# Performance work log

Measured on AMD Instinct MI355X. Metric: run time of the kernel, lower is better.

## Reference

```python
import jax, jax.numpy as jnp
import numpy as np

B, R, C = 32, 32, 32
NB, NC = 2, 20
CH = 6 + 2 * (R + C) + 2 * NC      # 174 label channels
CHP = NB * CH                      # 348 pred channels


def setup_inputs() -> dict:
    key = jax.random.key(0)
    pred = jax.random.uniform(key, (B, R, C, CHP), dtype=jnp.float32)
    rng = np.random.default_rng(0)
    label = rng.random((B, R, C, CH)).astype(np.float32)
    # object flag: exactly 1.0 where a center exists (the code tests == 1)
    label[..., 0] = (rng.random((B, R, C)) < 0.15).astype(np.float32)
    # one-hot corner row / col pointers
    rc = rng.integers(0, R, (B, R, C))
    cc = rng.integers(0, C, (B, R, C))
    label[..., 6:6 + R] = np.eye(R, dtype=np.float32)[rc]
    label[..., 6 + R:6 + R + C] = np.eye(C, dtype=np.float32)[cc]
    return {"pred": pred, "label": jnp.asarray(label), "num_box": NB, "num_class": NC}


def _take(a, idx):
    # gather one channel per cell; idx: [B,R,C] int
    return jnp.take_along_axis(a, idx[..., None], axis=-1)[..., 0]


def _convbox_match(pred, label, nb, nc):
    Bs, Rs, Cs, ch = label.shape
    chp = pred.shape[-1]
    base = 6 + 2 * (Rs + Cs)
    f32 = pred.dtype
    b_idx = jnp.arange(Bs)[:, None, None]
    rowm = jnp.broadcast_to(jnp.arange(Rs)[None, :, None], (Bs, Rs, Cs))
    colm = jnp.broadcast_to(jnp.arange(Cs)[None, None, :], (Bs, Rs, Cs))
    flag = (label[..., 0] == 1.0)
    rowc = jnp.argmax(label[..., 6:6 + Rs], axis=-1)            # first index of one-hot
    colc = jnp.argmax(label[..., 6 + Rs:6 + Rs + Cs], axis=-1)
    Lc = label[b_idx, rowc, colc]   # [B,R,C,ch]  values at corner cell
    Pc = pred[b_idx, rowc, colc]    # [B,R,C,chp]

    # ground-truth box per cell
    xm_t = (label[..., 2] + colm) / Cs
    ym_t = (label[..., 3] + rowm) / Rs
    xc_t = (Lc[..., 4] + colc) / Cs
    yc_t = (Lc[..., 5] + rowc) / Rs
    tw = jnp.abs(xm_t - xc_t) * 2.0
    th = jnp.abs(ym_t - yc_t) * 2.0

    scores = []
    for i in range(nb):
        sm = base * nb + i * nc
        sc = (base + nc) * nb + i * nc
        cat = (jnp.sum((pred[..., sm:sm + nc] - label[..., base:base + nc]) ** 2, -1)
               + jnp.sum((Pc[..., sc:sc + nc] - Lc[..., base + nc:base + 2 * nc]) ** 2, -1))
        conn_m = (_take(pred, 6 * nb + i * (Rs + Cs) + rowc)
                  * _take(pred, 6 * nb + i * (Rs + Cs) + Rs + colc))
        conn_c = (_take(Pc, (6 + Rs + Cs) * nb + i * (Rs + Cs) + rowm)
                  * _take(Pc, (6 + Rs + Cs) * nb + i * (Rs + Cs) + Rs + colm))
        conn = (conn_m + conn_c) / 2.0
        # faithful to source: channel index literally offset by colm / rowm
        xm_p = _take(pred, (nb + i) * 2 + 0 + colm) / Cs
        ym_p = _take(pred, (nb + i) * 2 + 1 + rowm) / Rs
        xc_p = _take(Pc, (nb * 2 + i) * 2 + 0 + colc) / Cs
        yc_p = _take(Pc, (nb * 2 + i) * 2 + 1 + rowc) / Rs
        ow = jnp.abs(xm_p - xc_p) * 2.0
        oh = jnp.abs(ym_p - yc_p) * 2.0
        w = jnp.minimum(xm_p + ow / 2, xm_t + tw / 2) - jnp.maximum(xm_p - ow / 2, xm_t - tw / 2)
        h = jnp.minimum(ym_p + oh / 2, ym_t + th / 2) - jnp.maximum(ym_p - oh / 2, ym_t - th / 2)
        inter = jnp.where((w < 0) | (h < 0), 0.0, w * h)
        union = ow * oh + tw * th - inter
        iou = inter / union
        rmse = (xm_p - xm_t) ** 2 + (ym_p - ym_t) ** 2 + (ow - tw) ** 2 + (oh - th) ** 2
        scores.append(conn * (iou - rmse + 0.1) + 0.1 * (2.0 - cat))
    best = jnp.argmax(jnp.stack(scores, axis=-1), axis=-1)  # [B,R,C] (first max, matches strict > update)

    val = flag.astype(f32)
    pred_mask = jnp.zeros((Bs, Rs, Cs, chp), f32)
    label_mask = jnp.zeros((Bs, Rs, Cs, ch), f32)
    ar_rc = jnp.arange(Rs + Cs)
    ar_nc = jnp.arange(nc)
    two = jnp.array([0, 1])
    bb = best[..., None]
    for n, (rt, ct) in enumerate([(rowm, colm), (rowc, colc)]):
        pch = jnp.concatenate([
            n * nb + bb,
            ((1 + n) * nb + bb) * 2 + two,
            (6 + n * (Rs + Cs)) * nb + bb * (Rs + Cs) + ar_rc,
            (base + n * nc) * nb + bb * nc + ar_nc,
        ], axis=-1)  # [B,R,C,3+R+C+nc]
        lch = jnp.concatenate([
            jnp.full((Bs, Rs, Cs, 1), n, dtype=jnp.int32),
            jnp.broadcast_to(2 * (1 + n) + two, (Bs, Rs, Cs, 2)),
            jnp.broadcast_to(6 + n * (Rs + Cs) + ar_rc, (Bs, Rs, Cs, Rs + Cs)),
            jnp.broadcast_to(base + n * nc + ar_nc, (Bs, Rs, Cs, nc)),
        ], axis=-1)
        # scatter 1s only at flagged cells; max() makes duplicates/overlaps a no-op
        pred_mask = pred_mask.at[b_idx[..., None], rt[..., None], ct[..., None], pch].max(val[..., None])
        label_mask = label_mask.at[b_idx[..., None], rt[..., None], ct[..., None], lch].max(val[..., None])
    return pred_mask, label_mask, label_mask


def reference(pred, label, num_box, num_class):
    return _convbox_match(pred, label, num_box, num_class)
```

## Files before the change

### kernel.cpp

```cpp
#include <hip/hip_runtime.h>

#define Bdim 32
#define Rdim 32
#define Cdim 32
#define NBOX 2
#define NCLS 20
#define CH   174
#define CHP  348
#define BASE 134

__global__ __launch_bounds__(256) void convbox_match_kernel(
    const float* __restrict__ pred, const float* __restrict__ label,
    float* __restrict__ out0,
    float* __restrict__ out1,
    float* __restrict__ out2)
{
    const int wave = (blockIdx.x << 2) | (threadIdx.x >> 6);
    const int lane = threadIdx.x & 63;
    const int c = wave & 31;
    const int r = (wave >> 5) & 31;
    const int b = wave >> 10;

    const float* Lcell = label + (size_t)wave * CH;

    if (Lcell[0] != 1.0f) return;

    float vr = (lane < 32) ? Lcell[6 + lane] : 0.0f;
    float vc = (lane < 32) ? Lcell[6 + 32 + lane] : 0.0f;
    unsigned long long mr = __ballot(lane < 32 && vr == 1.0f);
    unsigned long long mc = __ballot(lane < 32 && vc == 1.0f);
    const int rowc = mr ? (int)__builtin_ctzll(mr) : 0;
    const int colc = mc ? (int)__builtin_ctzll(mc) : 0;

    const int cornIdx = (b * Rdim + rowc) * Cdim + colc;
    const float* Lcorn = label + (size_t)cornIdx * CH;
    const float* Pcell = pred + (size_t)wave * CHP;
    const float* Pcorn = pred + (size_t)cornIdx * CHP;

    const float inv = 0.03125f;
    float xm_t = (Lcell[2] + (float)c) * inv;
    float ym_t = (Lcell[3] + (float)r) * inv;
    float xc_t = (Lcorn[4] + (float)colc) * inv;
    float yc_t = (Lcorn[5] + (float)rowc) * inv;
    float tw = fabsf(xm_t - xc_t) * 2.0f;
    float th = fabsf(ym_t - yc_t) * 2.0f;

    float score[NBOX];
#pragma unroll
    for (int i = 0; i < NBOX; ++i) {
        float cat = 0.0f;
#pragma unroll
        for (int k = 0; k < NCLS; ++k) {
            float d1 = Pcell[268 + i * NCLS + k] - Lcell[BASE + k];
            float d2 = Pcorn[308 + i * NCLS + k] - Lcorn[BASE + NCLS + k];
            cat += d1 * d1 + d2 * d2;
        }
        float conn_m = Pcell[12 + i * 64 + rowc] * Pcell[12 + i * 64 + 32 + colc];
        float conn_c = Pcorn[140 + i * 64 + r]   * Pcorn[140 + i * 64 + 32 + c];
        float conn = (conn_m + conn_c) * 0.5f;
        float xm_p = Pcell[(NBOX + i) * 2 + 0 + c] * inv;
        float ym_p = Pcell[(NBOX + i) * 2 + 1 + r] * inv;
        float xc_p = Pcorn[(NBOX * 2 + i) * 2 + 0 + colc] * inv;
        float yc_p = Pcorn[(NBOX * 2 + i) * 2 + 1 + rowc] * inv;
        float ow = fabsf(xm_p - xc_p) * 2.0f;
        float oh = fabsf(ym_p - yc_p) * 2.0f;
        float w = fminf(xm_p + ow * 0.5f, xm_t + tw * 0.5f)
                - fmaxf(xm_p - ow * 0.5f, xm_t - tw * 0.5f);
        float h = fminf(ym_p + oh * 0.5f, ym_t + th * 0.5f)
                - fmaxf(ym_p - oh * 0.5f, ym_t - th * 0.5f);
        float inter = (w < 0.0f || h < 0.0f) ? 0.0f : w * h;
        float uni = ow * oh + tw * th - inter;
        float iou = inter / uni;
        float rmse = (xm_p - xm_t) * (xm_p - xm_t) + (ym_p - ym_t) * (ym_p - ym_t)
                   + (ow - tw) * (ow - tw) + (oh - th) * (oh - th);
        score[i] = conn * (iou - rmse + 0.1f) + 0.1f * (2.0f - cat);
    }
    const int best = (score[1] > score[0]) ? 1 : 0;

#pragma unroll
    for (int n = 0; n < 2; ++n) {
        const int rt = n ? rowc : r;
        const int ct = n ? colc : c;
        const int tcell = (b * Rdim + rt) * Cdim + ct;

        float* pm = out0 + (size_t)tcell * CHP;
        if (lane == 0) pm[n * NBOX + best] = 1.0f;
        if (lane < 2)  pm[(1 + n) * NBOX * 2 + 2 * best + lane] = 1.0f;
        pm[(6 + n * 64) * NBOX + 64 * best + lane] = 1.0f;
        if (lane < NCLS) pm[(BASE + n * NCLS) * NBOX + NCLS * best + lane] = 1.0f;

        float* l1 = out1 + (size_t)tcell * CH;
        float* l2 = out2 + (size_t)tcell * CH;
        if (lane == 0) { l1[n] = 1.0f; l2[n] = 1.0f; }
        if (lane < 2)  { l1[2 * (1 + n) + lane] = 1.0f; l2[2 * (1 + n) + lane] = 1.0f; }
        l1[6 + n * 64 + lane] = 1.0f;
        l2[6 + n * 64 + lane] = 1.0f;
        if (lane < NCLS) { l1[BASE + n * NCLS + lane] = 1.0f; l2[BASE + n * NCLS + lane] = 1.0f; }
    }
}

extern "C" void kernel_launch(void* const* d_in, const int* in_sizes, int n_in,
                              void* d_out, int out_size, void* d_ws, size_t ws_size,
                              hipStream_t stream) {
    const float* pred  = (const float*)d_in[0];
    const float* label = (const float*)d_in[1];

    float* out0 = (float*)d_out;
    float* out1 = out0 + (size_t)Bdim * Rdim * Cdim * CHP;
    float* out2 = out1 + (size_t)Bdim * Rdim * Cdim * CH;

    hipMemsetAsync(d_out, 0, (size_t)out_size * sizeof(float), stream);

    const int n_cells = Bdim * Rdim * Cdim;
    const int blocks = n_cells / 4;
    convbox_match_kernel<<<blocks, 256, 0, stream>>>(pred, label, out0, out1, out2);
}
```

Baseline: 150.0 us.

## Replace full output memset plus scatter with gather-style dense mask writer

Splits the work into a match kernel that records each cell's best box and an atomic OR of corner hits into a workspace, and a write kernel that produces every output cell with vectorized stores. This drops the large memset of all three outputs and the scattered per-lane single-float writes, so each output byte is written exactly once. In exchange it adds a small workspace memset, an extra kernel launch, atomics on corner flags, and per-element range tests in the writer.

```diff
diff --git a/kernel.cpp b/kernel.cpp
--- a/kernel.cpp
+++ b/kernel.cpp
@@ -8,22 +8,38 @@
 #define CH   174
 #define CHP  348
 #define BASE 134
+#define NCELL (Bdim * Rdim * Cdim)
 
-__global__ __launch_bounds__(256) void convbox_match_kernel(
+__device__ __forceinline__ bool in_pred(int j, int n, int b) {
+    return (j == 2 * n + b)
+        || ((unsigned)(j - (4 + 4 * n + 2 * b)) < 2u)
+        || ((unsigned)(j - (12 + 128 * n + 64 * b)) < 64u)
+        || ((unsigned)(j - (268 + 40 * n + 20 * b)) < 20u);
+}
+
+__device__ __forceinline__ bool in_lab(int j, int n) {
+    return (j == n)
+        || ((unsigned)(j - (2 + 2 * n)) < 2u)
+        || ((unsigned)(j - (6 + 64 * n)) < 64u)
+        || ((unsigned)(j - (134 + 20 * n)) < 20u);
+}
+
+__global__ __launch_bounds__(256) void match_kernel(
     const float* __restrict__ pred, const float* __restrict__ label,
-    float* __restrict__ out0,
-    float* __restrict__ out1,
-    float* __restrict__ out2)
+    int* __restrict__ flagbest, int* __restrict__ corner)
 {
-    const int wave = (blockIdx.x << 2) | (threadIdx.x >> 6);
+    const int cell = (blockIdx.x << 2) | (threadIdx.x >> 6);
     const int lane = threadIdx.x & 63;
-    const int c = wave & 31;
-    const int r = (wave >> 5) & 31;
-    const int b = wave >> 10;
+    const int c = cell & 31;
+    const int r = (cell >> 5) & 31;
+    const int b = cell >> 10;
 
-    const float* Lcell = label + (size_t)wave * CH;
+    const float* Lcell = label + (size_t)cell * CH;
 
-    if (Lcell[0] != 1.0f) return;
+    if (Lcell[0] != 1.0f) {
+        if (lane == 0) flagbest[cell] = 0;
+        return;
+    }
 
     float vr = (lane < 32) ? Lcell[6 + lane] : 0.0f;
     float vc = (lane < 32) ? Lcell[6 + 32 + lane] : 0.0f;
@@ -34,7 +50,7 @@
 
     const int cornIdx = (b * Rdim + rowc) * Cdim + colc;
     const float* Lcorn = label + (size_t)cornIdx * CH;
-    const float* Pcell = pred + (size_t)wave * CHP;
+    const float* Pcell = pred + (size_t)cell * CHP;
     const float* Pcorn = pred + (size_t)cornIdx * CHP;
 
     const float inv = 0.03125f;
@@ -77,25 +93,58 @@
     }
     const int best = (score[1] > score[0]) ? 1 : 0;
 
+    if (lane == 0) {
+        flagbest[cell] = 1 + best;
+        atomicOr(&corner[cornIdx], 1 << best);
+    }
+}
+
+__global__ __launch_bounds__(256) void write_kernel(
+    const int* __restrict__ flagbest, const int* __restrict__ corner,
+    float* __restrict__ out0, float* __restrict__ out1, float* __restrict__ out2)
+{
+    const int cell = (blockIdx.x << 2) | (threadIdx.x >> 6);
+    const int lane = threadIdx.x & 63;
+
+    const int fb = flagbest[cell];
+    const int cb = corner[cell];
+
+    float4* __restrict__ o0 = (float4*)(out0 + (size_t)cell * CHP);
+    float2* __restrict__ o1 = (float2*)(out1 + (size_t)cell * CH);
+    float2* __restrict__ o2 = (float2*)(out2 + (size_t)cell * CH);
+
+    if ((fb | cb) == 0) {
+        const float4 z4 = make_float4(0.f, 0.f, 0.f, 0.f);
+        const float2 z2 = make_float2(0.f, 0.f);
+        for (int t = lane; t < 87; t += 64) { o0[t] = z4; o1[t] = z2; o2[t] = z2; }
+        return;
+    }
+
+    const bool flag = fb > 0;
+    const int  b0   = flag ? fb - 1 : 0;
+    const bool c0   = (cb & 1) != 0;
+    const bool c1   = (cb & 2) != 0;
+    const bool anyc = c0 | c1;
+
+    for (int t = lane; t < 87; t += 64) {
+        float4 v;
+        float* vp = (float*)&v;
 #pragma unroll
-    for (int n = 0; n < 2; ++n) {
-        const int rt = n ? rowc : r;
-        const int ct = n ? colc : c;
-        const int tcell = (b * Rdim + rt) * Cdim + ct;
+        for (int e = 0; e < 4; ++e) {
+            const int j = 4 * t + e;
+            const bool x = (flag && in_pred(j, 0, b0))
+                        || (c0   && in_pred(j, 1, 0))
+                        || (c1   && in_pred(j, 1, 1));
+            vp[e] = x ? 1.0f : 0.0f;
+        }
+        o0[t] = v;
 
-        float* pm = out0 + (size_t)tcell * CHP;
-        if (lane == 0) pm[n * NBOX + best] = 1.0f;
-        if (lane < 2)  pm[(1 + n) * NBOX * 2 + 2 * best + lane] = 1.0f;
-        pm[(6 + n * 64) * NBOX + 64 * best + lane] = 1.0f;
-        if (lane < NCLS) pm[(BASE + n * NCLS) * NBOX + NCLS * best + lane] = 1.0f;
-
-        float* l1 = out1 + (size_t)tcell * CH;
-        float* l2 = out2 + (size_t)tcell * CH;
-        if (lane == 0) { l1[n] = 1.0f; l2[n] = 1.0f; }
-        if (lane < 2)  { l1[2 * (1 + n) + lane] = 1.0f; l2[2 * (1 + n) + lane] = 1.0f; }
-        l1[6 + n * 64 + lane] = 1.0f;
-        l2[6 + n * 64 + lane] = 1.0f;
-        if (lane < NCLS) { l1[BASE + n * NCLS + lane] = 1.0f; l2[BASE + n * NCLS + lane] = 1.0f; }
+        const int k = 2 * t;
+        float2 u;
+        u.x = ((flag && in_lab(k,     0)) || (anyc && in_lab(k,     1))) ? 1.0f : 0.0f;
+        u.y = ((flag && in_lab(k + 1, 0)) || (anyc && in_lab(k + 1, 1))) ? 1.0f : 0.0f;
+        o1[t] = u;
+        o2[t] = u;
     }
 }
 
@@ -106,12 +155,15 @@
     const float* label = (const float*)d_in[1];
 
     float* out0 = (float*)d_out;
-    float* out1 = out0 + (size_t)Bdim * Rdim * Cdim * CHP;
-    float* out2 = out1 + (size_t)Bdim * Rdim * Cdim * CH;
+    float* out1 = out0 + (size_t)NCELL * CHP;
+    float* out2 = out1 + (size_t)NCELL * CH;
 
-    hipMemsetAsync(d_out, 0, (size_t)out_size * sizeof(float), stream);
+    int* flagbest = (int*)d_ws;
+    int* corner   = flagbest + NCELL;
 
-    const int n_cells = Bdim * Rdim * Cdim;
-    const int blocks = n_cells / 4;
-    convbox_match_kernel<<<blocks, 256, 0, stream>>>(pred, label, out0, out1, out2);
+    hipMemsetAsync(corner, 0, NCELL * sizeof(int), stream);
+
+    const int blocks = NCELL / 4;
+    match_kernel<<<blocks, 256, 0, stream>>>(pred, label, flagbest, corner);
+    write_kernel<<<blocks, 256, 0, stream>>>(flagbest, corner, out0, out1, out2);
 }
```

After: 157.6 us. +5.1%, slower.
